# Performance work log

Hardware: AMD Instinct MI355X
Metric: run time of the kernel (lower is better)

## Reference

```python
import jax, jax.numpy as jnp
import numpy as np

EPS = 0.3          # FAGCN eps residual coefficient
N_LAYERS = 2


def setup_inputs() -> dict:
    key = jax.random.key(0)
    ks = jax.random.split(key, 8)
    N, E, IN, H, OUT = 50000, 800000, 256, 64, 16
    return {
        "h": jax.random.normal(ks[0], (N, IN), dtype=jnp.float32),
        "src": jax.random.randint(ks[1], (E,), 0, N, dtype=jnp.int32),
        "dst": jax.random.randint(ks[2], (E,), 0, N, dtype=jnp.int32),
        "t1_w": jax.random.normal(ks[3], (H, IN), dtype=jnp.float32) * (1.414 / np.sqrt(IN)),
        "t1_b": jnp.zeros((H,), dtype=jnp.float32),
        "gate_w": jax.random.normal(ks[4], (N_LAYERS, 2 * H), dtype=jnp.float32) * (1.414 / np.sqrt(2 * H)),
        "gate_b": jnp.zeros((N_LAYERS,), dtype=jnp.float32),
        "t2_w": jax.random.normal(ks[5], (OUT, H), dtype=jnp.float32) * (1.414 / np.sqrt(H)),
        "t2_b": jnp.zeros((OUT,), dtype=jnp.float32),
    }


def reference(h, src, dst, t1_w, t1_b, gate_w, gate_b, t2_w, t2_b):
    N = h.shape[0]
    # symmetric degree norm d = in_degree^-0.5 (as in FAGCN preprocessing)
    deg = jnp.zeros((N,), dtype=h.dtype).at[dst].add(1.0)
    d = jax.lax.rsqrt(jnp.maximum(deg, 1.0))

    # t1 + relu (dropout is identity in eval mode)
    x = jax.nn.relu(h @ t1_w.T + t1_b)          # [N, H]
    raw = x
    for l in range(N_LAYERS):
        hs = x[src]                              # [E, H] gathered src feats
        hd = x[dst]                              # [E, H] gathered dst feats
        # gate(concat[dst, src]) -> tanh -> scalar per edge
        g = jnp.tanh(jnp.concatenate([hd, hs], axis=-1) @ gate_w[l] + gate_b[l])  # [E]
        e = g * d[dst] * d[src]                  # [E]
        msg = hs * e[:, None]                    # [E, H]
        z = jax.ops.segment_sum(msg, dst, num_segments=N)  # scatter-sum to dst
        x = EPS * raw + z

    logits = x @ t2_w.T + t2_b                   # [N, OUT]
    return jax.nn.log_softmax(logits, axis=-1)
```

## Files before the change

kernel.cpp:

```cpp
#include <hip/hip_runtime.h>
#include <math.h>

#define EPS 0.3f
#define CAP 64
#define SPILLCAP 65536

typedef __attribute__((ext_vector_type(8))) short bf16x8;
typedef __attribute__((ext_vector_type(4))) float f32x4;

__device__ __forceinline__ short f2bf(float f) {
    union { float f; unsigned u; } v; v.f = f;
    unsigned r = v.u + 0x7FFFu + ((v.u >> 16) & 1u);
    return (short)(r >> 16);
}
__device__ __forceinline__ float bf2f(short s) {
    union { unsigned u; float f; } v;
    v.u = ((unsigned)(unsigned short)s) << 16;
    return v.f;
}
__device__ __forceinline__ int f2bf_pk(float lo, float hi) {
#if __has_builtin(__builtin_amdgcn_cvt_pk_bf16_f32)
    auto r = __builtin_amdgcn_cvt_pk_bf16_f32(lo, hi);
    int out; __builtin_memcpy(&out, &r, 4);
    return out;
#else
    return ((int)(unsigned short)f2bf(lo)) | (((int)(unsigned short)f2bf(hi)) << 16);
#endif
}
__device__ __forceinline__ float fast_tanh(float x) {
    return 1.0f - 2.0f / (1.0f + __expf(2.0f * x));
}


__global__ __launch_bounds__(256) void init_k(const float* __restrict__ w,
                                              short* __restrict__ wb,
                                              int* __restrict__ cnt,
                                              int* __restrict__ spillN, int N) {
    int bid = blockIdx.x, tid = threadIdx.x;
    if (bid < 64) wb[bid * 256 + tid] = f2bf(w[bid * 256 + tid]);
    for (int i = bid * 256 + tid; i < N; i += gridDim.x * 256) cnt[i] = 0;
    if (bid == 0 && tid == 0) *spillN = 0;
}

#define LROW 264
__global__ __launch_bounds__(256) void scatter_t1(
    const int* __restrict__ src, const int* __restrict__ dst, int E,
    int* __restrict__ cnt, unsigned short* __restrict__ esrc2,
    unsigned* __restrict__ spill, int* __restrict__ spillN,
    const float* __restrict__ h, const short* __restrict__ wb,
    const float* __restrict__ t1b, const float* __restrict__ gw,
    short* __restrict__ XAh, float* __restrict__ ga0, float* __restrict__ gb0,
    int N, int SCB)
{
    __shared__ short lds[4][16 * LROW];
    int tid = threadIdx.x;

    if ((int)blockIdx.x < SCB) {
        for (int i = blockIdx.x * 256 + tid; i < E; i += SCB * 256) {
            int d = dst[i];
            int slot = atomicAdd(&cnt[d], 1);
            if (slot < CAP) {
                esrc2[(size_t)d * CAP + slot] = (unsigned short)src[i];
            } else {
                int sp = atomicAdd(spillN, 1);
                if (sp < SPILLCAP)
                    spill[sp] = ((unsigned)d << 16) | (unsigned)(src[i] & 0xFFFF);
            }
        }
        return;
    }

    int bid = blockIdx.x - SCB;
    int wave = tid >> 6;
    int lane = tid & 63;
    int l15 = lane & 15, quad = lane >> 4;
    int M0 = (bid * 4 + wave) * 16;
    if (M0 >= N) return;
    int rlim = N - M0;

    short* myl = lds[wave];
    const float* hb = h + (size_t)M0 * 256;
    #pragma unroll
    for (int r = 0; r < 16; ++r) {
        if (r < rlim) {
            float4 v = *(const float4*)&hb[(size_t)r * 256 + lane * 4];
            int2 sv; sv.x = f2bf_pk(v.x, v.y); sv.y = f2bf_pk(v.z, v.w);
            *(int2*)&myl[r * LROW + lane * 4] = sv;
        }
    }

    f32x4 acc[4];
    #pragma unroll
    for (int nt = 0; nt < 4; ++nt) acc[nt] = (f32x4){0.f, 0.f, 0.f, 0.f};

    const short* wq = wb + quad * 8;
    #pragma unroll
    for (int kc = 0; kc < 256; kc += 32) {
        bf16x8 af = *(const bf16x8*)&myl[l15 * LROW + kc + quad * 8];
        #pragma unroll
        for (int nt = 0; nt < 4; ++nt) {
            bf16x8 bf = *(const bf16x8*)(wq + (size_t)(nt * 16 + l15) * 256 + kc);
            acc[nt] = __builtin_amdgcn_mfma_f32_16x16x32_bf16(af, bf, acc[nt], 0, 0, 0);
        }
    }

    float pa[4] = {0.f, 0.f, 0.f, 0.f};
    float pb[4] = {0.f, 0.f, 0.f, 0.f};
    #pragma unroll
    for (int nt = 0; nt < 4; ++nt) {
        int n = nt * 16 + l15;
        float bias = t1b[n];
        float gd = gw[n], gs = gw[64 + n];
        #pragma unroll
        for (int r = 0; r < 4; ++r) {
            int row = quad * 4 + r;
            if (row < rlim) {
                float x = fmaxf(acc[nt][r] + bias, 0.f);
                XAh[(size_t)(M0 + row) * 64 + n] = f2bf(x);
                pa[r] += x * gd;
                pb[r] += x * gs;
            }
        }
    }
    #pragma unroll
    for (int off = 1; off < 16; off <<= 1) {
        #pragma unroll
        for (int r = 0; r < 4; ++r) {
            pa[r] += __shfl_xor(pa[r], off, 64);
            pb[r] += __shfl_xor(pb[r], off, 64);
        }
    }
    if (l15 == 0) {
        #pragma unroll
        for (int r = 0; r < 4; ++r) {
            int row = quad * 4 + r;
            if (row < rlim) {
                ga0[M0 + row] = pa[r];
                gb0[M0 + row] = pb[r];
            }
        }
    }
}

__device__ __forceinline__ void gather_core3(
    const int* __restrict__ cnt, const unsigned short* __restrict__ esrc2,
    const float* __restrict__ a, const float* __restrict__ gb,
    const unsigned* __restrict__ spill, const int* __restrict__ spillN,
    const short* __restrict__ xch, const short* __restrict__ rawh,
    float gbias, int t, int lane, float acc[8])
{
    int g = (lane >> 3) & 3;
    int l = lane & 7;
    int j = lane & 31;
    int hbase = lane & 32;

    int deg = cnt[t];
    int degrow = min(deg, CAP);
    int beg = t * CAP;
    float atg = a[t] + gbias;
    float dt = rsqrtf(fmaxf((float)deg, 1.0f));

    int ev = (j < degrow) ? (int)esrc2[beg + j] : 0;
    float gbe = gb[ev];
    float ce = (float)cnt[ev];
    float cv = fast_tanh(atg + gbe) * dt * rsqrtf(fmaxf(ce, 1.0f));

    int sarr[8]; float carr[8];
    #pragma unroll
    for (int k = 0; k < 8; ++k) {
        int srcl = hbase + g + 4 * k;
        sarr[k] = __shfl(ev, srcl, 64);
        carr[k] = __shfl(cv, srcl, 64);
    }

    #pragma unroll
    for (int k = 0; k < 8; ++k) acc[k] = 0.f;
    if (g == 0) {
        bf16x8 rv = *(const bf16x8*)&rawh[(size_t)t * 64 + l * 8];
        #pragma unroll
        for (int k = 0; k < 8; ++k) acc[k] = EPS * bf2f(rv[k]);
    }

    int lim = min(degrow, 32);
    #pragma unroll
    for (int k = 0; k < 8; ++k) {
        if (g + 4 * k < lim) {
            int s0 = sarr[k];
            float c0 = carr[k];
            bf16x8 x0 = *(const bf16x8*)&xch[(size_t)s0 * 64 + l * 8];
            #pragma unroll
            for (int kk = 0; kk < 8; ++kk) acc[kk] += c0 * bf2f(x0[kk]);
        }
    }
    for (int i = beg + 32 + g; i < beg + degrow; i += 4) {
        int s0 = (int)esrc2[i];
        float c0 = fast_tanh(atg + gb[s0]) * dt * rsqrtf(fmaxf((float)cnt[s0], 1.f));
        bf16x8 x0 = *(const bf16x8*)&xch[(size_t)s0 * 64 + l * 8];
        #pragma unroll
        for (int k = 0; k < 8; ++k) acc[k] += c0 * bf2f(x0[k]);
    }
    int sn = min(*spillN, SPILLCAP);
    if (sn > 0) {
        for (int i = 0; i < sn; ++i) {
            unsigned e = spill[i];
            if ((int)(e >> 16) == t && g == 0) {
                int s0 = (int)(e & 0xFFFFu);
                float c0 = fast_tanh(atg + gb[s0]) * dt * rsqrtf(fmaxf((float)cnt[s0], 1.f));
                bf16x8 x0 = *(const bf16x8*)&xch[(size_t)s0 * 64 + l * 8];
                #pragma unroll
                for (int k = 0; k < 8; ++k) acc[k] += c0 * bf2f(x0[k]);
            }
        }
    }

    #pragma unroll
    for (int off = 8; off < 32; off <<= 1) {
        #pragma unroll
        for (int k = 0; k < 8; ++k) acc[k] += __shfl_xor(acc[k], off, 64);
    }
}

__global__ __launch_bounds__(256) void gather_mid(
    const int* __restrict__ cnt, const unsigned short* __restrict__ esrc2,
    const float* __restrict__ a, const float* __restrict__ gb,
    const unsigned* __restrict__ spill, const int* __restrict__ spillN,
    const short* __restrict__ xch, const float* __restrict__ gbp,
    short* __restrict__ xnh, const float* __restrict__ gw_next,
    float* __restrict__ ga_next, float* __restrict__ gb_next, int N)
{
    int tid = threadIdx.x;
    int t = blockIdx.x * 8 + (tid >> 5);
    int tt = min(t, N - 1);
    bool valid = (t < N);
    int lane = tid & 63;
    int g = (lane >> 3) & 3, l = lane & 7;
    float acc[8];
    gather_core3(cnt, esrc2, a, gb, spill, spillN, xch, xch, gbp[0], tt, lane, acc);

    if (g == 0 && valid) {
        int4 o;
        o.x = f2bf_pk(acc[0], acc[1]); o.y = f2bf_pk(acc[2], acc[3]);
        o.z = f2bf_pk(acc[4], acc[5]); o.w = f2bf_pk(acc[6], acc[7]);
        *(int4*)&xnh[(size_t)tt * 64 + l * 8] = o;
    }
    float av = 0.f, bv = 0.f;
    #pragma unroll
    for (int k = 0; k < 8; ++k) {
        av += acc[k] * gw_next[l * 8 + k];
        bv += acc[k] * gw_next[64 + l * 8 + k];
    }
    #pragma unroll
    for (int off = 1; off < 8; off <<= 1) {
        av += __shfl_xor(av, off, 64);
        bv += __shfl_xor(bv, off, 64);
    }
    if ((lane & 31) == 0 && valid) {
        ga_next[tt] = av;
        gb_next[tt] = bv;
    }
}

__global__ __launch_bounds__(256) void gather_out(
    const int* __restrict__ cnt, const unsigned short* __restrict__ esrc2,
    const float* __restrict__ a, const float* __restrict__ gb,
    const unsigned* __restrict__ spill, const int* __restrict__ spillN,
    const short* __restrict__ xch, const short* __restrict__ rawh,
    const float* __restrict__ gbp, const float* __restrict__ t2w,
    const float* __restrict__ t2b, float* __restrict__ out, int N)
{
    int tid = threadIdx.x;
    int t = blockIdx.x * 8 + (tid >> 5);
    int tt = min(t, N - 1);
    bool valid = (t < N);
    int lane = tid & 63;
    int g = (lane >> 3) & 3, l = lane & 7;
    float acc[8];
    gather_core3(cnt, esrc2, a, gb, spill, spillN, xch, rawh, gbp[1], tt, lane, acc);

    int j0 = 4 * g;
    float p[4];
    #pragma unroll
    for (int i = 0; i < 4; ++i) {
        const float* w = &t2w[(size_t)(j0 + i) * 64 + l * 8];
        float s = 0.f;
        #pragma unroll
        for (int k = 0; k < 8; ++k) s += acc[k] * w[k];
        p[i] = s;
    }
    #pragma unroll
    for (int off = 1; off < 8; off <<= 1) {
        #pragma unroll
        for (int i = 0; i < 4; ++i) p[i] += __shfl_xor(p[i], off, 64);
    }
    float li[4];
    #pragma unroll
    for (int i = 0; i < 4; ++i) li[i] = p[i] + t2b[j0 + i];
    float m = fmaxf(fmaxf(li[0], li[1]), fmaxf(li[2], li[3]));
    #pragma unroll
    for (int off = 8; off < 32; off <<= 1) m = fmaxf(m, __shfl_xor(m, off, 64));
    float s = 0.f;
    #pragma unroll
    for (int i = 0; i < 4; ++i) s += __expf(li[i] - m);
    #pragma unroll
    for (int off = 8; off < 32; off <<= 1) s += __shfl_xor(s, off, 64);
    float lse = m + __logf(s);
    if (l == 0 && valid) {
        float4 o;
        o.x = li[0] - lse; o.y = li[1] - lse;
        o.z = li[2] - lse; o.w = li[3] - lse;
        *(float4*)&out[(size_t)tt * 16 + j0] = o;
    }
}

extern "C" void kernel_launch(void* const* d_in, const int* in_sizes, int n_in,
                              void* d_out, int out_size, void* d_ws, size_t ws_size,
                              hipStream_t stream) {
    const float* h    = (const float*)d_in[0];
    const int*   src  = (const int*)d_in[1];
    const int*   dst  = (const int*)d_in[2];
    const float* t1w  = (const float*)d_in[3];
    const float* t1b  = (const float*)d_in[4];
    const float* gw   = (const float*)d_in[5];
    const float* gbia = (const float*)d_in[6];
    const float* t2w  = (const float*)d_in[7];
    const float* t2b  = (const float*)d_in[8];
    float* out = (float*)d_out;

    int N = in_sizes[0] / 256;
    int E = in_sizes[1];

    char* p = (char*)d_ws;
    short*    XAh    = (short*)p;       p += (size_t)N * 64 * 2;
    short*    XBh    = (short*)p;       p += (size_t)N * 64 * 2;
    float*    ga0    = (float*)p;       p += (size_t)N * 4;
    float*    ga1    = (float*)p;       p += (size_t)N * 4;
    float*    gb0    = (float*)p;       p += (size_t)N * 4;
    float*    gb1    = (float*)p;       p += (size_t)N * 4;
    int*      cnt    = (int*)p;         p += (size_t)N * 4;
    int*      spillN = (int*)p;         p += 16;
    unsigned* spill  = (unsigned*)p;    p += (size_t)SPILLCAP * 4;
    p = (char*)(((size_t)p + 15) & ~(size_t)15);
    unsigned short* esrc2 = (unsigned short*)p; p += (size_t)N * CAP * 2;
    p = (char*)(((size_t)p + 15) & ~(size_t)15);
    short*    wbf    = (short*)p;

    init_k<<<256, 256, 0, stream>>>(t1w, wbf, cnt, spillN, N);

    int SCB = 240;
    scatter_t1<<<SCB + (N + 63) / 64, 256, 0, stream>>>(
        src, dst, E, cnt, esrc2, spill, spillN,
        h, wbf, t1b, gw, XAh, ga0, gb0, N, SCB);

    gather_mid<<<(N + 7) / 8, 256, 0, stream>>>(cnt, esrc2, ga0, gb0, spill, spillN,
                                                XAh, gbia, XBh, gw + 128, ga1, gb1, N);

    gather_out<<<(N + 7) / 8, 256, 0, stream>>>(cnt, esrc2, ga1, gb1, spill, spillN,
                                                XBh, XAh, gbia, t2w, t2b, out, N);
}
```

Before: 205.4 us.

## Partition scatter and gather work by XCD to keep node ranges L2-local

```diff
diff --git a/kernel.cpp b/kernel.cpp
--- a/kernel.cpp
+++ b/kernel.cpp
@@ -4,6 +4,7 @@
 #define EPS 0.3f
 #define CAP 64
 #define SPILLCAP 65536
+#define NXCD 8
 
 typedef __attribute__((ext_vector_type(8))) short bf16x8;
 typedef __attribute__((ext_vector_type(4))) float f32x4;
@@ -31,7 +32,6 @@
     return 1.0f - 2.0f / (1.0f + __expf(2.0f * x));
 }
 
-
 __global__ __launch_bounds__(256) void init_k(const float* __restrict__ w,
                                               short* __restrict__ wb,
                                               int* __restrict__ cnt,
@@ -50,21 +50,28 @@
     const float* __restrict__ h, const short* __restrict__ wb,
     const float* __restrict__ t1b, const float* __restrict__ gw,
     short* __restrict__ XAh, float* __restrict__ ga0, float* __restrict__ gb0,
-    int N, int SCB)
+    int N, int SCB, int NX)
 {
     __shared__ short lds[4][16 * LROW];
     int tid = threadIdx.x;
 
     if ((int)blockIdx.x < SCB) {
-        for (int i = blockIdx.x * 256 + tid; i < E; i += SCB * 256) {
+        int x  = blockIdx.x & (NXCD - 1);
+        int r  = blockIdx.x >> 3;
+        int nb = SCB >> 3;
+        int lo = x * NX, hi = min(lo + NX, N);
+        for (int i = r * 256 + tid; i < E; i += nb * 256) {
             int d = dst[i];
-            int slot = atomicAdd(&cnt[d], 1);
-            if (slot < CAP) {
-                esrc2[(size_t)d * CAP + slot] = (unsigned short)src[i];
-            } else {
-                int sp = atomicAdd(spillN, 1);
-                if (sp < SPILLCAP)
-                    spill[sp] = ((unsigned)d << 16) | (unsigned)(src[i] & 0xFFFF);
+            if (d >= lo && d < hi) {
+                int s = src[i];
+                int slot = atomicAdd(&cnt[d], 1);
+                if (slot < CAP) {
+                    esrc2[(size_t)d * CAP + slot] = (unsigned short)s;
+                } else {
+                    int sp = atomicAdd(spillN, 1);
+                    if (sp < SPILLCAP)
+                        spill[sp] = ((unsigned)d << 16) | ((unsigned)s & 0xFFFFu);
+                }
             }
         }
         return;
@@ -142,45 +149,41 @@
     }
 }
 
-__device__ __forceinline__ void gather_core3(
+__device__ __forceinline__ void gather_core4(
     const int* __restrict__ cnt, const unsigned short* __restrict__ esrc2,
     const float* __restrict__ a, const float* __restrict__ gb,
     const unsigned* __restrict__ spill, const int* __restrict__ spillN,
     const short* __restrict__ xch, const short* __restrict__ rawh,
-    float gbias, int t, int lane, float acc[8])
+    float gbias, int t, int lane, int N, float fin[8])
 {
     int g = (lane >> 3) & 3;
     int l = lane & 7;
     int j = lane & 31;
     int hbase = lane & 32;
 
+    int beg = t * CAP;
+    int ev_raw = (int)esrc2[beg + j];
     int deg = cnt[t];
-    int degrow = min(deg, CAP);
-    int beg = t * CAP;
     float atg = a[t] + gbias;
-    float dt = rsqrtf(fmaxf((float)deg, 1.0f));
-
-    int ev = (j < degrow) ? (int)esrc2[beg + j] : 0;
-    float gbe = gb[ev];
-    float ce = (float)cnt[ev];
-    float cv = fast_tanh(atg + gbe) * dt * rsqrtf(fmaxf(ce, 1.0f));
+
+    int evc = min(ev_raw, N - 1);
+    float gbe = gb[evc];
+    float ce = (float)cnt[evc];
+    float cv = fast_tanh(atg + gbe) * rsqrtf(fmaxf(ce, 1.0f));
 
     int sarr[8]; float carr[8];
     #pragma unroll
     for (int k = 0; k < 8; ++k) {
         int srcl = hbase + g + 4 * k;
-        sarr[k] = __shfl(ev, srcl, 64);
+        sarr[k] = __shfl(evc, srcl, 64);
         carr[k] = __shfl(cv, srcl, 64);
     }
 
+    float acc[8];
     #pragma unroll
     for (int k = 0; k < 8; ++k) acc[k] = 0.f;
-    if (g == 0) {
-        bf16x8 rv = *(const bf16x8*)&rawh[(size_t)t * 64 + l * 8];
-        #pragma unroll
-        for (int k = 0; k < 8; ++k) acc[k] = EPS * bf2f(rv[k]);
-    }
-
+
+    int degrow = min(deg, CAP);
     int lim = min(degrow, 32);
     #pragma unroll
     for (int k = 0; k < 8; ++k) {
@@ -194,7 +197,7 @@
     }
     for (int i = beg + 32 + g; i < beg + degrow; i += 4) {
         int s0 = (int)esrc2[i];
-        float c0 = fast_tanh(atg + gb[s0]) * dt * rsqrtf(fmaxf((float)cnt[s0], 1.f));
+        float c0 = fast_tanh(atg + gb[s0]) * rsqrtf(fmaxf((float)cnt[s0], 1.f));
         bf16x8 x0 = *(const bf16x8*)&xch[(size_t)s0 * 64 + l * 8];
         #pragma unroll
         for (int k = 0; k < 8; ++k) acc[k] += c0 * bf2f(x0[k]);
@@ -205,7 +208,7 @@
             unsigned e = spill[i];
             if ((int)(e >> 16) == t && g == 0) {
                 int s0 = (int)(e & 0xFFFFu);
-                float c0 = fast_tanh(atg + gb[s0]) * dt * rsqrtf(fmaxf((float)cnt[s0], 1.f));
+                float c0 = fast_tanh(atg + gb[s0]) * rsqrtf(fmaxf((float)cnt[s0], 1.f));
                 bf16x8 x0 = *(const bf16x8*)&xch[(size_t)s0 * 64 + l * 8];
                 #pragma unroll
                 for (int k = 0; k < 8; ++k) acc[k] += c0 * bf2f(x0[k]);
@@ -218,6 +221,23 @@
         #pragma unroll
         for (int k = 0; k < 8; ++k) acc[k] += __shfl_xor(acc[k], off, 64);
     }
+
+    float dt = rsqrtf(fmaxf((float)deg, 1.0f));
+    bf16x8 rv = *(const bf16x8*)&rawh[(size_t)t * 64 + l * 8];
+    #pragma unroll
+    for (int k = 0; k < 8; ++k) fin[k] = EPS * bf2f(rv[k]) + dt * acc[k];
+}
+
+__device__ __forceinline__ void node_map(int bid, int tid, int N, int NX,
+                                         int& t, int& tt, bool& valid) {
+    int x = bid & (NXCD - 1);
+    int q = bid >> 3;
+    int ln = q * 8 + (tid >> 5);
+    t = x * NX + ln;
+    int hi = min(x * NX + NX, N);
+    valid = (ln < NX) && (t < hi);
+    int fb = max(hi - 1, 0);
+    tt = valid ? t : fb;
 }
 
 __global__ __launch_bounds__(256) void gather_mid(
@@ -226,28 +246,27 @@
     const unsigned* __restrict__ spill, const int* __restrict__ spillN,
     const short* __restrict__ xch, const float* __restrict__ gbp,
     short* __restrict__ xnh, const float* __restrict__ gw_next,
-    float* __restrict__ ga_next, float* __restrict__ gb_next, int N)
+    float* __restrict__ ga_next, float* __restrict__ gb_next, int N, int NX)
 {
     int tid = threadIdx.x;
-    int t = blockIdx.x * 8 + (tid >> 5);
-    int tt = min(t, N - 1);
-    bool valid = (t < N);
+    int t, tt; bool valid;
+    node_map(blockIdx.x, tid, N, NX, t, tt, valid);
     int lane = tid & 63;
     int g = (lane >> 3) & 3, l = lane & 7;
-    float acc[8];
-    gather_core3(cnt, esrc2, a, gb, spill, spillN, xch, xch, gbp[0], tt, lane, acc);
+    float fin[8];
+    gather_core4(cnt, esrc2, a, gb, spill, spillN, xch, xch, gbp[0], tt, lane, N, fin);
 
     if (g == 0 && valid) {
         int4 o;
-        o.x = f2bf_pk(acc[0], acc[1]); o.y = f2bf_pk(acc[2], acc[3]);
-        o.z = f2bf_pk(acc[4], acc[5]); o.w = f2bf_pk(acc[6], acc[7]);
+        o.x = f2bf_pk(fin[0], fin[1]); o.y = f2bf_pk(fin[2], fin[3]);
+        o.z = f2bf_pk(fin[4], fin[5]); o.w = f2bf_pk(fin[6], fin[7]);
         *(int4*)&xnh[(size_t)tt * 64 + l * 8] = o;
     }
     float av = 0.f, bv = 0.f;
     #pragma unroll
     for (int k = 0; k < 8; ++k) {
-        av += acc[k] * gw_next[l * 8 + k];
-        bv += acc[k] * gw_next[64 + l * 8 + k];
+        av += fin[k] * gw_next[l * 8 + k];
+        bv += fin[k] * gw_next[64 + l * 8 + k];
     }
     #pragma unroll
     for (int off = 1; off < 8; off <<= 1) {
@@ -266,16 +285,15 @@
     const unsigned* __restrict__ spill, const int* __restrict__ spillN,
     const short* __restrict__ xch, const short* __restrict__ rawh,
     const float* __restrict__ gbp, const float* __restrict__ t2w,
-    const float* __restrict__ t2b, float* __restrict__ out, int N)
+    const float* __restrict__ t2b, float* __restrict__ out, int N, int NX)
 {
     int tid = threadIdx.x;
-    int t = blockIdx.x * 8 + (tid >> 5);
-    int tt = min(t, N - 1);
-    bool valid = (t < N);
+    int t, tt; bool valid;
+    node_map(blockIdx.x, tid, N, NX, t, tt, valid);
     int lane = tid & 63;
     int g = (lane >> 3) & 3, l = lane & 7;
-    float acc[8];
-    gather_core3(cnt, esrc2, a, gb, spill, spillN, xch, rawh, gbp[1], tt, lane, acc);
+    float fin[8];
+    gather_core4(cnt, esrc2, a, gb, spill, spillN, xch, rawh, gbp[1], tt, lane, N, fin);
 
     int j0 = 4 * g;
     float p[4];
@@ -284,7 +302,7 @@
         const float* w = &t2w[(size_t)(j0 + i) * 64 + l * 8];
         float s = 0.f;
         #pragma unroll
-        for (int k = 0; k < 8; ++k) s += acc[k] * w[k];
+        for (int k = 0; k < 8; ++k) s += fin[k] * w[k];
         p[i] = s;
     }
     #pragma unroll
@@ -328,6 +346,7 @@
 
     int N = in_sizes[0] / 256;
     int E = in_sizes[1];
+    int NX = (N + NXCD - 1) / NXCD;
 
     char* p = (char*)d_ws;
     short*    XAh    = (short*)p;       p += (size_t)N * 64 * 2;
@@ -349,11 +368,13 @@
     int SCB = 240;
     scatter_t1<<<SCB + (N + 63) / 64, 256, 0, stream>>>(
         src, dst, E, cnt, esrc2, spill, spillN,
-        h, wbf, t1b, gw, XAh, ga0, gb0, N, SCB);
-
-    gather_mid<<<(N + 7) / 8, 256, 0, stream>>>(cnt, esrc2, ga0, gb0, spill, spillN,
-                                                XAh, gbia, XBh, gw + 128, ga1, gb1, N);
-
-    gather_out<<<(N + 7) / 8, 256, 0, stream>>>(cnt, esrc2, ga1, gb1, spill, spillN,
-                                                XBh, XAh, gbia, t2w, t2b, out, N);
-}
+        h, wbf, t1b, gw, XAh, ga0, gb0, N, SCB, NX);
+
+    int PB = (NX + 7) / 8;
+    gather_mid<<<NXCD * PB, 256, 0, stream>>>(cnt, esrc2, ga0, gb0, spill, spillN,
+                                              XAh, gbia, XBh, gw + 128, ga1, gb1,
+                                              N, NX);
+
+    gather_out<<<NXCD * PB, 256, 0, stream>>>(cnt, esrc2, ga1, gb1, spill, spillN,
+                                              XBh, XAh, gbia, t2w, t2b, out, N, NX);
+}
```

Result: slower. 238.3 us (+16.1%).

## Split feature gathers into two 32-column halves to shrink random-access working set

Applied to the files above, without the earlier changes.

```diff
diff --git a/kernel.cpp b/kernel.cpp
--- a/kernel.cpp
+++ b/kernel.cpp
@@ -6,6 +6,7 @@
 #define SPILLCAP 65536
 
 typedef __attribute__((ext_vector_type(8))) short bf16x8;
+typedef __attribute__((ext_vector_type(4))) short bf16x4;
 typedef __attribute__((ext_vector_type(4))) float f32x4;
 
 __device__ __forceinline__ short f2bf(float f) {
@@ -31,7 +32,6 @@
     return 1.0f - 2.0f / (1.0f + __expf(2.0f * x));
 }
 
-
 __global__ __launch_bounds__(256) void init_k(const float* __restrict__ w,
                                               short* __restrict__ wb,
                                               int* __restrict__ cnt,
@@ -49,7 +49,8 @@
     unsigned* __restrict__ spill, int* __restrict__ spillN,
     const float* __restrict__ h, const short* __restrict__ wb,
     const float* __restrict__ t1b, const float* __restrict__ gw,
-    short* __restrict__ XAh, float* __restrict__ ga0, float* __restrict__ gb0,
+    short* __restrict__ XA0, short* __restrict__ XA1,
+    float* __restrict__ ga0, float* __restrict__ gb0,
     int N, int SCB)
 {
     __shared__ short lds[4][16 * LROW];
@@ -64,7 +65,7 @@
             } else {
                 int sp = atomicAdd(spillN, 1);
                 if (sp < SPILLCAP)
-                    spill[sp] = ((unsigned)d << 16) | (unsigned)(src[i] & 0xFFFF);
+                    spill[sp] = ((unsigned)d << 16) | ((unsigned)src[i] & 0xFFFFu);
             }
         }
         return;
@@ -109,6 +110,8 @@
     #pragma unroll
     for (int nt = 0; nt < 4; ++nt) {
         int n = nt * 16 + l15;
+        short* xd = (nt < 2) ? XA0 : XA1;
+        int nn = n & 31;
         float bias = t1b[n];
         float gd = gw[n], gs = gw[64 + n];
         #pragma unroll
@@ -116,7 +119,7 @@
             int row = quad * 4 + r;
             if (row < rlim) {
                 float x = fmaxf(acc[nt][r] + bias, 0.f);
-                XAh[(size_t)(M0 + row) * 64 + n] = f2bf(x);
+                xd[(size_t)(M0 + row) * 32 + nn] = f2bf(x);
                 pa[r] += x * gd;
                 pb[r] += x * gs;
             }
@@ -142,62 +145,64 @@
     }
 }
 
-__device__ __forceinline__ void gather_core3(
+template <int PASS>
+__device__ __forceinline__ void gather_half(
     const int* __restrict__ cnt, const unsigned short* __restrict__ esrc2,
     const float* __restrict__ a, const float* __restrict__ gb,
+    short* __restrict__ cbuf,
     const unsigned* __restrict__ spill, const int* __restrict__ spillN,
-    const short* __restrict__ xch, const short* __restrict__ rawh,
-    float gbias, int t, int lane, float acc[8])
+    const short* __restrict__ xh, const short* __restrict__ rawh,
+    float gbias, int t, int lane, int N, float fin[4])
 {
     int g = (lane >> 3) & 3;
     int l = lane & 7;
     int j = lane & 31;
     int hbase = lane & 32;
 
+    int beg = t * CAP;
+    int ev_raw = (int)__builtin_nontemporal_load(&esrc2[beg + j]);
     int deg = cnt[t];
-    int degrow = min(deg, CAP);
-    int beg = t * CAP;
     float atg = a[t] + gbias;
-    float dt = rsqrtf(fmaxf((float)deg, 1.0f));
-
-    int ev = (j < degrow) ? (int)esrc2[beg + j] : 0;
-    float gbe = gb[ev];
-    float ce = (float)cnt[ev];
-    float cv = fast_tanh(atg + gbe) * dt * rsqrtf(fmaxf(ce, 1.0f));
+    int evc = min(ev_raw, N - 1);
+
+    float cv;
+    if (PASS == 0) {
+        float gbe = gb[evc];
+        float ce  = (float)cnt[evc];
+        float cf = fast_tanh(atg + gbe) * rsqrtf(fmaxf(ce, 1.0f));
+        short ch = f2bf(cf);
+        cbuf[t * 32 + j] = ch;
+        cv = bf2f(ch);
+    } else {
+        cv = bf2f(cbuf[t * 32 + j]);
+    }
 
     int sarr[8]; float carr[8];
     #pragma unroll
     for (int k = 0; k < 8; ++k) {
         int srcl = hbase + g + 4 * k;
-        sarr[k] = __shfl(ev, srcl, 64);
+        sarr[k] = __shfl(evc, srcl, 64);
         carr[k] = __shfl(cv, srcl, 64);
     }
 
-    #pragma unroll
-    for (int k = 0; k < 8; ++k) acc[k] = 0.f;
-    if (g == 0) {
-        bf16x8 rv = *(const bf16x8*)&rawh[(size_t)t * 64 + l * 8];
-        #pragma unroll
-        for (int k = 0; k < 8; ++k) acc[k] = EPS * bf2f(rv[k]);
-    }
-
+    float acc[4] = {0.f, 0.f, 0.f, 0.f};
+    int degrow = min(deg, CAP);
     int lim = min(degrow, 32);
     #pragma unroll
     for (int k = 0; k < 8; ++k) {
         if (g + 4 * k < lim) {
-            int s0 = sarr[k];
+            bf16x4 x0 = *(const bf16x4*)&xh[(size_t)sarr[k] * 32 + l * 4];
             float c0 = carr[k];
-            bf16x8 x0 = *(const bf16x8*)&xch[(size_t)s0 * 64 + l * 8];
             #pragma unroll
-            for (int kk = 0; kk < 8; ++kk) acc[kk] += c0 * bf2f(x0[kk]);
+            for (int kk = 0; kk < 4; ++kk) acc[kk] += c0 * bf2f(x0[kk]);
         }
     }
     for (int i = beg + 32 + g; i < beg + degrow; i += 4) {
         int s0 = (int)esrc2[i];
-        float c0 = fast_tanh(atg + gb[s0]) * dt * rsqrtf(fmaxf((float)cnt[s0], 1.f));
-        bf16x8 x0 = *(const bf16x8*)&xch[(size_t)s0 * 64 + l * 8];
-        #pragma unroll
-        for (int k = 0; k < 8; ++k) acc[k] += c0 * bf2f(x0[k]);
+        float c0 = fast_tanh(atg + gb[s0]) * rsqrtf(fmaxf((float)cnt[s0], 1.f));
+        bf16x4 x0 = *(const bf16x4*)&xh[(size_t)s0 * 32 + l * 4];
+        #pragma unroll
+        for (int k = 0; k < 4; ++k) acc[k] += c0 * bf2f(x0[k]);
     }
     int sn = min(*spillN, SPILLCAP);
     if (sn > 0) {
@@ -205,10 +210,10 @@
             unsigned e = spill[i];
             if ((int)(e >> 16) == t && g == 0) {
                 int s0 = (int)(e & 0xFFFFu);
-                float c0 = fast_tanh(atg + gb[s0]) * dt * rsqrtf(fmaxf((float)cnt[s0], 1.f));
-                bf16x8 x0 = *(const bf16x8*)&xch[(size_t)s0 * 64 + l * 8];
+                float c0 = fast_tanh(atg + gb[s0]) * rsqrtf(fmaxf((float)cnt[s0], 1.f));
+                bf16x4 x0 = *(const bf16x4*)&xh[(size_t)s0 * 32 + l * 4];
                 #pragma unroll
-                for (int k = 0; k < 8; ++k) acc[k] += c0 * bf2f(x0[k]);
+                for (int k = 0; k < 4; ++k) acc[k] += c0 * bf2f(x0[k]);
             }
         }
     }
@@ -216,16 +221,24 @@
     #pragma unroll
     for (int off = 8; off < 32; off <<= 1) {
         #pragma unroll
-        for (int k = 0; k < 8; ++k) acc[k] += __shfl_xor(acc[k], off, 64);
-    }
-}
-
-__global__ __launch_bounds__(256) void gather_mid(
+        for (int k = 0; k < 4; ++k) acc[k] += __shfl_xor(acc[k], off, 64);
+    }
+
+    float dt = rsqrtf(fmaxf((float)deg, 1.0f));
+    bf16x4 rv = *(const bf16x4*)&rawh[(size_t)t * 32 + l * 4];
+    #pragma unroll
+    for (int k = 0; k < 4; ++k) fin[k] = EPS * bf2f(rv[k]) + dt * acc[k];
+}
+
+template <int PASS>
+__global__ __launch_bounds__(256) void gather_mid_k(
     const int* __restrict__ cnt, const unsigned short* __restrict__ esrc2,
     const float* __restrict__ a, const float* __restrict__ gb,
+    short* __restrict__ cbuf,
     const unsigned* __restrict__ spill, const int* __restrict__ spillN,
-    const short* __restrict__ xch, const float* __restrict__ gbp,
+    const short* __restrict__ xh, const float* __restrict__ gbp,
     short* __restrict__ xnh, const float* __restrict__ gw_next,
+    float* __restrict__ paA, float* __restrict__ pbA,
     float* __restrict__ ga_next, float* __restrict__ gb_next, int N)
 {
     int tid = threadIdx.x;
@@ -234,20 +247,20 @@
     bool valid = (t < N);
     int lane = tid & 63;
     int g = (lane >> 3) & 3, l = lane & 7;
-    float acc[8];
-    gather_core3(cnt, esrc2, a, gb, spill, spillN, xch, xch, gbp[0], tt, lane, acc);
+    float fin[4];
+    gather_half<PASS>(cnt, esrc2, a, gb, cbuf, spill, spillN, xh, xh,
+                      gbp[0], tt, lane, N, fin);
 
     if (g == 0 && valid) {
-        int4 o;
-        o.x = f2bf_pk(acc[0], acc[1]); o.y = f2bf_pk(acc[2], acc[3]);
-        o.z = f2bf_pk(acc[4], acc[5]); o.w = f2bf_pk(acc[6], acc[7]);
-        *(int4*)&xnh[(size_t)tt * 64 + l * 8] = o;
+        int2 o;
+        o.x = f2bf_pk(fin[0], fin[1]); o.y = f2bf_pk(fin[2], fin[3]);
+        *(int2*)&xnh[(size_t)tt * 32 + l * 4] = o;
     }
     float av = 0.f, bv = 0.f;
     #pragma unroll
-    for (int k = 0; k < 8; ++k) {
-        av += acc[k] * gw_next[l * 8 + k];
-        bv += acc[k] * gw_next[64 + l * 8 + k];
+    for (int k = 0; k < 4; ++k) {
+        av += fin[k] * gw_next[PASS * 32 + l * 4 + k];
+        bv += fin[k] * gw_next[64 + PASS * 32 + l * 4 + k];
     }
     #pragma unroll
     for (int off = 1; off < 8; off <<= 1) {
@@ -255,18 +268,21 @@
         bv += __shfl_xor(bv, off, 64);
     }
     if ((lane & 31) == 0 && valid) {
-        ga_next[tt] = av;
-        gb_next[tt] = bv;
-    }
-}
-
-__global__ __launch_bounds__(256) void gather_out(
+        if (PASS == 0) { paA[tt] = av;           pbA[tt] = bv; }
+        else           { ga_next[tt] = paA[tt] + av; gb_next[tt] = pbA[tt] + bv; }
+    }
+}
+
+template <int PASS>
+__global__ __launch_bounds__(256) void gather_out_k(
     const int* __restrict__ cnt, const unsigned short* __restrict__ esrc2,
     const float* __restrict__ a, const float* __restrict__ gb,
+    short* __restrict__ cbuf,
     const unsigned* __restrict__ spill, const int* __restrict__ spillN,
-    const short* __restrict__ xch, const short* __restrict__ rawh,
+    const short* __restrict__ xh, const short* __restrict__ rawh,
     const float* __restrict__ gbp, const float* __restrict__ t2w,
-    const float* __restrict__ t2b, float* __restrict__ out, int N)
+    const float* __restrict__ t2b, float* __restrict__ plogit,
+    float* __restrict__ out, int N)
 {
     int tid = threadIdx.x;
     int t = blockIdx.x * 8 + (tid >> 5);
@@ -274,17 +290,18 @@
     bool valid = (t < N);
     int lane = tid & 63;
     int g = (lane >> 3) & 3, l = lane & 7;
-    float acc[8];
-    gather_core3(cnt, esrc2, a, gb, spill, spillN, xch, rawh, gbp[1], tt, lane, acc);
+    float fin[4];
+    gather_half<PASS>(cnt, esrc2, a, gb, cbuf, spill, spillN, xh, rawh,
+                      gbp[1], tt, lane, N, fin);
 
     int j0 = 4 * g;
     float p[4];
     #pragma unroll
     for (int i = 0; i < 4; ++i) {
-        const float* w = &t2w[(size_t)(j0 + i) * 64 + l * 8];
+        const float* w = &t2w[(size_t)(j0 + i) * 64 + PASS * 32 + l * 4];
         float s = 0.f;
         #pragma unroll
-        for (int k = 0; k < 8; ++k) s += acc[k] * w[k];
+        for (int k = 0; k < 4; ++k) s += fin[k] * w[k];
         p[i] = s;
     }
     #pragma unroll
@@ -292,23 +309,34 @@
         #pragma unroll
         for (int i = 0; i < 4; ++i) p[i] += __shfl_xor(p[i], off, 64);
     }
-    float li[4];
-    #pragma unroll
-    for (int i = 0; i < 4; ++i) li[i] = p[i] + t2b[j0 + i];
-    float m = fmaxf(fmaxf(li[0], li[1]), fmaxf(li[2], li[3]));
-    #pragma unroll
-    for (int off = 8; off < 32; off <<= 1) m = fmaxf(m, __shfl_xor(m, off, 64));
-    float s = 0.f;
-    #pragma unroll
-    for (int i = 0; i < 4; ++i) s += __expf(li[i] - m);
-    #pragma unroll
-    for (int off = 8; off < 32; off <<= 1) s += __shfl_xor(s, off, 64);
-    float lse = m + __logf(s);
-    if (l == 0 && valid) {
-        float4 o;
-        o.x = li[0] - lse; o.y = li[1] - lse;
-        o.z = li[2] - lse; o.w = li[3] - lse;
-        *(float4*)&out[(size_t)tt * 16 + j0] = o;
+
+    if (PASS == 0) {
+        if (l == 0 && valid) {
+            float4 o; o.x = p[0]; o.y = p[1]; o.z = p[2]; o.w = p[3];
+            *(float4*)&plogit[(size_t)tt * 16 + j0] = o;
+        }
+    } else {
+        float4 pr = *(const float4*)&plogit[(size_t)tt * 16 + j0];
+        float li[4];
+        li[0] = p[0] + pr.x + t2b[j0 + 0];
+        li[1] = p[1] + pr.y + t2b[j0 + 1];
+        li[2] = p[2] + pr.z + t2b[j0 + 2];
+        li[3] = p[3] + pr.w + t2b[j0 + 3];
+        float m = fmaxf(fmaxf(li[0], li[1]), fmaxf(li[2], li[3]));
+        #pragma unroll
+        for (int off = 8; off < 32; off <<= 1) m = fmaxf(m, __shfl_xor(m, off, 64));
+        float s = 0.f;
+        #pragma unroll
+        for (int i = 0; i < 4; ++i) s += __expf(li[i] - m);
+        #pragma unroll
+        for (int off = 8; off < 32; off <<= 1) s += __shfl_xor(s, off, 64);
+        float lse = m + __logf(s);
+        if (l == 0 && valid) {
+            float4 o;
+            o.x = li[0] - lse; o.y = li[1] - lse;
+            o.z = li[2] - lse; o.w = li[3] - lse;
+            *(float4*)&out[(size_t)tt * 16 + j0] = o;
+        }
     }
 }
 
@@ -330,18 +358,25 @@
     int E = in_sizes[1];
 
     char* p = (char*)d_ws;
-    short*    XAh    = (short*)p;       p += (size_t)N * 64 * 2;
-    short*    XBh    = (short*)p;       p += (size_t)N * 64 * 2;
+    short*    XA0    = (short*)p;       p += (size_t)N * 32 * 2;
+    short*    XA1    = (short*)p;       p += (size_t)N * 32 * 2;
+    short*    XB0    = (short*)p;       p += (size_t)N * 32 * 2;
+    short*    XB1    = (short*)p;       p += (size_t)N * 32 * 2;
     float*    ga0    = (float*)p;       p += (size_t)N * 4;
     float*    ga1    = (float*)p;       p += (size_t)N * 4;
     float*    gb0    = (float*)p;       p += (size_t)N * 4;
     float*    gb1    = (float*)p;       p += (size_t)N * 4;
+    float*    paA    = (float*)p;       p += (size_t)N * 4;
+    float*    pbA    = (float*)p;       p += (size_t)N * 4;
+    float*    plogit = (float*)p;       p += (size_t)N * 16 * 4;
     int*      cnt    = (int*)p;         p += (size_t)N * 4;
     int*      spillN = (int*)p;         p += 16;
     unsigned* spill  = (unsigned*)p;    p += (size_t)SPILLCAP * 4;
     p = (char*)(((size_t)p + 15) & ~(size_t)15);
     unsigned short* esrc2 = (unsigned short*)p; p += (size_t)N * CAP * 2;
     p = (char*)(((size_t)p + 15) & ~(size_t)15);
+    short*    cbuf   = (short*)p;       p += (size_t)N * 32 * 2;
+    p = (char*)(((size_t)p + 15) & ~(size_t)15);
     short*    wbf    = (short*)p;
 
     init_k<<<256, 256, 0, stream>>>(t1w, wbf, cnt, spillN, N);
@@ -349,11 +384,17 @@
     int SCB = 240;
     scatter_t1<<<SCB + (N + 63) / 64, 256, 0, stream>>>(
         src, dst, E, cnt, esrc2, spill, spillN,
-        h, wbf, t1b, gw, XAh, ga0, gb0, N, SCB);
-
-    gather_mid<<<(N + 7) / 8, 256, 0, stream>>>(cnt, esrc2, ga0, gb0, spill, spillN,
-                                                XAh, gbia, XBh, gw + 128, ga1, gb1, N);
-
-    gather_out<<<(N + 7) / 8, 256, 0, stream>>>(cnt, esrc2, ga1, gb1, spill, spillN,
-                                                XBh, XAh, gbia, t2w, t2b, out, N);
-}
+        h, wbf, t1b, gw, XA0, XA1, ga0, gb0, N, SCB);
+
+    int GB = (N + 7) / 8;
+    gather_mid_k<0><<<GB, 256, 0, stream>>>(cnt, esrc2, ga0, gb0, cbuf, spill, spillN,
+                                            XA0, gbia, XB0, gw + 128, paA, pbA,
+                                            ga1, gb1, N);
+    gather_mid_k<1><<<GB, 256, 0, stream>>>(cnt, esrc2, ga0, gb0, cbuf, spill, spillN,
+                                            XA1, gbia, XB1, gw + 128, paA, pbA,
+                                            ga1, gb1, N);
+    gather_out_k<0><<<GB, 256, 0, stream>>>(cnt, esrc2, ga1, gb1, cbuf, spill, spillN,
+                                            XB0, XA0, gbia, t2w, t2b, plogit, out, N);
+    gather_out_k<1><<<GB, 256, 0, stream>>>(cnt, esrc2, ga1, gb1, cbuf, spill, spillN,
+                                            XB1, XA1, gbia, t2w, t2b, plogit, out, N);
+}
```

Result: slower. 230.5 us (+12.3%).
